# Performance work log

Measured on AMD Instinct MI355X. Metric: run time of the kernel, lower is better.

## Reference

```python
import jax, jax.numpy as jnp
import numpy as np

T, N, F = 8, 128, 128


def setup_inputs() -> dict:
    key = jax.random.key(0)
    k1, k2, k3, k4 = jax.random.split(key, 4)
    node_feats = jax.random.normal(k1, (T, N, F), dtype=jnp.float32)
    edge_feats = jax.random.normal(k2, (T, N, N, F), dtype=jnp.float32)
    # Conv3d(in=3, out=1, kernel=1) weights flattened to 3 scalars + bias
    w = jax.random.normal(k3, (3,), dtype=jnp.float32)
    b = jax.random.normal(k4, (1,), dtype=jnp.float32)
    return {"node_feats": node_feats, "edge_feats": edge_feats, "w": w, "b": b}


def reference(node_feats, edge_feats, w, b):
    # node_feats: [T, N, F]; edge_feats: [T, N, N, F]
    x_i = node_feats[:, :, None, :]          # [T, N, 1, F] -> broadcast over j
    x_ij = x_i - node_feats[:, None, :, :]    # [T, N, N, F]  (x_i - x_j)
    # fused 1x1x1 conv over the 3 stacked channels + bias, then tanh
    e = jnp.tanh(w[0] * x_i + w[1] * x_ij + w[2] * edge_feats + b[0])  # [T, N, N, F]
    n = e.shape[1]
    diag_mask = (1.0 - jnp.eye(n, dtype=e.dtype))[None, :, :, None]
    e = e * diag_mask
    # original returns transpose(1,3) of [T,F,i,j] -> [T,j,i,F]: swap i and j
    return jnp.swapaxes(e, 1, 2)
```

## Files before the change

kernel.cpp:

```cpp
#include <hip/hip_runtime.h>


__device__ __forceinline__ float fast_tanh(float x) {
    x = fminf(fmaxf(x, -9.0f), 9.0f);
    float t = __expf(2.0f * x);
    return (t - 1.0f) / (t + 1.0f);
}

__global__ __launch_bounds__(256)
void EdgeUpdateNetwork_44555990729422_kernel(
    const float* __restrict__ node,
    const float* __restrict__ edge,
    const float* __restrict__ w,
    const float* __restrict__ b,
    float* __restrict__ out,
    int total_vec)
{
    const float w1  = w[1];
    const float w01 = w[0] + w1;
    const float w2  = w[2];
    const float bb  = b[0];

    const float4* __restrict__ edge4 = reinterpret_cast<const float4*>(edge);
    const float4* __restrict__ node4 = reinterpret_cast<const float4*>(node);
    float4* __restrict__ out4        = reinterpret_cast<float4*>(out);

    int idx    = blockIdx.x * blockDim.x + threadIdx.x;
    int stride = gridDim.x * blockDim.x;

    for (int v = idx; v < total_vec; v += stride) {
        int f4 = v & 31;
        int i  = (v >> 5)  & 127;
        int j  = (v >> 12) & 127;
        int t  = v >> 19;

        float4 e4 = edge4[(((t << 7) + i) << 7 | j) * 32 + f4];
        float4 ni = node4[((t << 7) + i) * 32 + f4];
        float4 nj = node4[((t << 7) + j) * 32 + f4];

        float m = (i == j) ? 0.0f : 1.0f;

        float4 r;
        r.x = m * fast_tanh(fmaf(w01, ni.x, fmaf(-w1, nj.x, fmaf(w2, e4.x, bb))));
        r.y = m * fast_tanh(fmaf(w01, ni.y, fmaf(-w1, nj.y, fmaf(w2, e4.y, bb))));
        r.z = m * fast_tanh(fmaf(w01, ni.z, fmaf(-w1, nj.z, fmaf(w2, e4.z, bb))));
        r.w = m * fast_tanh(fmaf(w01, ni.w, fmaf(-w1, nj.w, fmaf(w2, e4.w, bb))));

        out4[v] = r;
    }
}

extern "C" void kernel_launch(void* const* d_in, const int* in_sizes, int n_in,
                              void* d_out, int out_size, void* d_ws, size_t ws_size,
                              hipStream_t stream) {
    const float* node = (const float*)d_in[0];
    const float* edge = (const float*)d_in[1];
    const float* w    = (const float*)d_in[2];
    const float* b    = (const float*)d_in[3];
    float* out        = (float*)d_out;

    const int total_vec = out_size / 4;
    const int block = 256;
    int blocks = (total_vec + block - 1) / block;
    if (blocks > 2048) blocks = 2048;

    EdgeUpdateNetwork_44555990729422_kernel<<<blocks, block, 0, stream>>>(
        node, edge, w, b, out, total_vec);
}
```

Baseline: 27.51 us.

## Tile 8x8 (i,j) blocks through shared memory with nontemporal stores

Replaces the grid-stride flat loop with one block per (t, 8x8 i/j tile). Each thread hoists its node_j term into constants, computes 8 rows into an LDS tile, then writes the transposed tile with nontemporal stores. The aim is to cut repeated node loads and index arithmetic and to keep output writes streaming. In exchange it adds 32KB of LDS per block and a barrier, and it hardcodes the grid size to the T=8, N=128 shape.

Result: faster. 26.23 us (-4.7%).

```diff
diff --git a/kernel.cpp b/kernel.cpp
--- a/kernel.cpp
+++ b/kernel.cpp
@@ -1,5 +1,7 @@
 #include <hip/hip_runtime.h>
 
+
+typedef float f32x4 __attribute__((ext_vector_type(4)));
 
 __device__ __forceinline__ float fast_tanh(float x) {
     x = fminf(fmaxf(x, -9.0f), 9.0f);
@@ -13,40 +15,58 @@
     const float* __restrict__ edge,
     const float* __restrict__ w,
     const float* __restrict__ b,
-    float* __restrict__ out,
-    int total_vec)
+    float* __restrict__ out)
 {
+    __shared__ f32x4 tile[8 * 8 * 32];
+
     const float w1  = w[1];
     const float w01 = w[0] + w1;
     const float w2  = w[2];
     const float bb  = b[0];
 
-    const float4* __restrict__ edge4 = reinterpret_cast<const float4*>(edge);
-    const float4* __restrict__ node4 = reinterpret_cast<const float4*>(node);
-    float4* __restrict__ out4        = reinterpret_cast<float4*>(out);
+    const int blk = blockIdx.x;
+    const int jb  = blk & 15;
+    const int ib  = (blk >> 4) & 15;
+    const int t   = blk >> 8;
+    const int i0  = ib << 3;
+    const int j0  = jb << 3;
 
-    int idx    = blockIdx.x * blockDim.x + threadIdx.x;
-    int stride = gridDim.x * blockDim.x;
+    const int tid = threadIdx.x;
+    const int f4  = tid & 31;
+    const int dq  = tid >> 5;
 
-    for (int v = idx; v < total_vec; v += stride) {
-        int f4 = v & 31;
-        int i  = (v >> 5)  & 127;
-        int j  = (v >> 12) & 127;
-        int t  = v >> 19;
+    const f32x4* __restrict__ node4 = reinterpret_cast<const f32x4*>(node);
+    const f32x4* __restrict__ edge4 = reinterpret_cast<const f32x4*>(edge);
+    f32x4* __restrict__ out4        = reinterpret_cast<f32x4*>(out);
 
-        float4 e4 = edge4[(((t << 7) + i) << 7 | j) * 32 + f4];
-        float4 ni = node4[((t << 7) + i) * 32 + f4];
-        float4 nj = node4[((t << 7) + j) * 32 + f4];
+    f32x4 nj = node4[((t << 7) + j0 + dq) * 32 + f4];
+    const float cx = fmaf(-w1, nj.x, bb);
+    const float cy = fmaf(-w1, nj.y, bb);
+    const float cz = fmaf(-w1, nj.z, bb);
+    const float cw = fmaf(-w1, nj.w, bb);
 
-        float m = (i == j) ? 0.0f : 1.0f;
+    #pragma unroll
+    for (int r = 0; r < 8; ++r) {
+        const int i = i0 + r;
+        f32x4 ni = node4[((t << 7) + i) * 32 + f4];
+        f32x4 e  = edge4[(((t << 7) + i) * 128 + j0 + dq) * 32 + f4];
+        const float m = (i == j0 + dq) ? 0.0f : 1.0f;
+        f32x4 rv;
+        rv.x = m * fast_tanh(fmaf(w01, ni.x, fmaf(w2, e.x, cx)));
+        rv.y = m * fast_tanh(fmaf(w01, ni.y, fmaf(w2, e.y, cy)));
+        rv.z = m * fast_tanh(fmaf(w01, ni.z, fmaf(w2, e.z, cz)));
+        rv.w = m * fast_tanh(fmaf(w01, ni.w, fmaf(w2, e.w, cw)));
+        tile[(dq * 8 + r) * 32 + f4] = rv;
+    }
 
-        float4 r;
-        r.x = m * fast_tanh(fmaf(w01, ni.x, fmaf(-w1, nj.x, fmaf(w2, e4.x, bb))));
-        r.y = m * fast_tanh(fmaf(w01, ni.y, fmaf(-w1, nj.y, fmaf(w2, e4.y, bb))));
-        r.z = m * fast_tanh(fmaf(w01, ni.z, fmaf(-w1, nj.z, fmaf(w2, e4.z, bb))));
-        r.w = m * fast_tanh(fmaf(w01, ni.w, fmaf(-w1, nj.w, fmaf(w2, e4.w, bb))));
+    __syncthreads();
 
-        out4[v] = r;
+    #pragma unroll
+    for (int r = 0; r < 8; ++r) {
+        f32x4 v = tile[(r * 8 + dq) * 32 + f4];
+        const int j = j0 + r;
+        __builtin_nontemporal_store(
+            v, &out4[(((t << 7) + j) * 128 + i0 + dq) * 32 + f4]);
     }
 }
 
@@ -59,11 +79,6 @@
     const float* b    = (const float*)d_in[3];
     float* out        = (float*)d_out;
 
-    const int total_vec = out_size / 4;
-    const int block = 256;
-    int blocks = (total_vec + block - 1) / block;
-    if (blocks > 2048) blocks = 2048;
-
-    EdgeUpdateNetwork_44555990729422_kernel<<<blocks, block, 0, stream>>>(
-        node, edge, w, b, out, total_vec);
+    EdgeUpdateNetwork_44555990729422_kernel<<<2048, 256, 0, stream>>>(
+        node, edge, w, b, out);
 }
```
